# Optimization experiments

Measured on AMD Instinct MI355X. Metric: run time of the kernel, lower is better.

The kernel has to match this reference:

```python
import jax, jax.numpy as jnp
import numpy as np


def setup_inputs() -> dict:
    key = jax.random.key(0)
    k1, k2, k3, k4 = jax.random.split(key, 4)
    C, R = 64, 8  # channels, reduced = channels // 8
    B, D, H, W = 2, 16, 16, 16
    x = jax.random.normal(k1, (B, C, D, H, W), dtype=jnp.float32)
    # 1x1x1 Conv3d kernels are plain [out_ch, in_ch] matrices (no bias)
    Wq = jax.random.normal(k2, (R, C), dtype=jnp.float32) * (C ** -0.5)
    Wk = jax.random.normal(k3, (R, C), dtype=jnp.float32) * (C ** -0.5)
    Wv = jax.random.normal(k4, (C, C), dtype=jnp.float32) * (C ** -0.5)
    gamma = jnp.ones((1,), dtype=jnp.float32) * 0.5  # nonzero so output depends on attention
    return {"x": x, "Wq": Wq, "Wk": Wk, "Wv": Wv, "gamma": gamma}


def reference(x, Wq, Wk, Wv, gamma):
    b, c, d, h, w = x.shape
    n = d * h * w
    xf = x.astype(jnp.float32).reshape(b, c, n)        # [b, c, n]
    q = jnp.einsum('rc,bcn->bnr', Wq, xf)              # [b, n, r]
    k = jnp.einsum('rc,bcn->brn', Wk, xf)              # [b, r, n]
    scale = q.shape[-1] ** -0.5
    attn = jax.nn.softmax(jnp.einsum('bnr,brm->bnm', q, k) * scale, axis=-1)  # [b, n_q, n_k]
    v = jnp.einsum('oc,bcn->bon', Wv, xf)              # [b, c, n]
    # out = value @ attn^T : out[b,c,q] = sum_k v[b,c,k] * attn[b,q,k]
    out = jnp.einsum('bck,bqk->bcq', v, attn).reshape(b, c, d, h, w)
    return x + gamma.astype(x.dtype) * out.astype(x.dtype)
```

## Files before the change

### kernel.cpp

```cpp
#include <hip/hip_runtime.h>
#include <math.h>

#define BB 2
#define CC 64
#define NN 4096
#define SCALE 0.35355339059327373f
#define DEFER_THR 8.0f

typedef _Float16 f16x8 __attribute__((ext_vector_type(8)));
typedef _Float16 f16x4 __attribute__((ext_vector_type(4)));
typedef float f32x4 __attribute__((ext_vector_type(4)));
typedef float f32x4v __attribute__((ext_vector_type(4)));

__global__ __launch_bounds__(256) void proj_kernel(
    const float* __restrict__ x, const float* __restrict__ Wq,
    const float* __restrict__ Wk, _Float16* __restrict__ qh,
    _Float16* __restrict__ kh, _Float16* __restrict__ xp)
{
    const int t = (int)blockIdx.x * 256 + (int)threadIdx.x;

    if (t < 16384) {
        const int grp = t >> 13;
        const int p = t & 8191;
        const int b = p >> 12;
        const int n = p & (NN - 1);
        const float* xc0 = x + (size_t)b * CC * NN + n;
        float xc[CC];
#pragma unroll
        for (int c = 0; c < CC; ++c) xc[c] = xc0[(size_t)c * NN];

        const float* W = (grp == 0) ? Wq : Wk;
        float a[8];
#pragma unroll
        for (int j = 0; j < 8; ++j) a[j] = 0.f;
#pragma unroll
        for (int c = 0; c < CC; ++c) {
            const float xv = xc[c];
#pragma unroll
            for (int j = 0; j < 8; ++j)
                a[j] = fmaf(W[j * CC + c], xv, a[j]);
        }
        f16x8 o;
        if (grp == 0) {
#pragma unroll
            for (int j = 0; j < 8; ++j) o[j] = (_Float16)(a[j] * SCALE);
            *(f16x8*)(qh + (size_t)p * 8) = o;
        } else {
#pragma unroll
            for (int j = 0; j < 8; ++j) o[j] = (_Float16)a[j];
            *(f16x8*)(kh + (size_t)p * 8) = o;
        }
    } else {
        const int pt = t - 16384;
        const int b = pt >> 15;
        const int g = (pt >> 6) & 511;
        const int c = pt & 63;
        const float* src = x + ((size_t)(b * CC + c) * NN + g * 8);
        const float4 a0 = *(const float4*)(src);
        const float4 a1 = *(const float4*)(src + 4);
        f16x8 o;
        o[0] = (_Float16)a0.x; o[1] = (_Float16)a0.y;
        o[2] = (_Float16)a0.z; o[3] = (_Float16)a0.w;
        o[4] = (_Float16)a1.x; o[5] = (_Float16)a1.y;
        o[6] = (_Float16)a1.z; o[7] = (_Float16)a1.w;
        ((f16x8*)xp)[pt] = o;
    }
}

static __device__ inline f16x8 make_pf(const float* p8, int lg, int lc)
{
    union { f16x4 h; unsigned u[2]; } P0, P1;
#pragma unroll
    for (int v = 0; v < 4; ++v) {
        P0.h[v] = (_Float16)p8[v];
        P1.h[v] = (_Float16)p8[4 + v];
    }
    const int sA = (((2 * lg) & 3) << 4) + lc;
    const int sB = (((2 * lg + 1) & 3) << 4) + lc;
    const unsigned t00 = __shfl(P0.u[0], sA), t01 = __shfl(P0.u[1], sA);
    const unsigned t10 = __shfl(P1.u[0], sA), t11 = __shfl(P1.u[1], sA);
    const unsigned u00 = __shfl(P0.u[0], sB), u01 = __shfl(P0.u[1], sB);
    const unsigned u10 = __shfl(P1.u[0], sB), u11 = __shfl(P1.u[1], sB);
    const bool hi = (lg & 2) != 0;
    union { unsigned u[4]; f16x8 v; } PF;
    PF.u[0] = hi ? t10 : t00;
    PF.u[1] = hi ? t11 : t01;
    PF.u[2] = hi ? u10 : u00;
    PF.u[3] = hi ? u11 : u01;
    return PF.v;
}

__global__ __launch_bounds__(512) void attn_kernel(
    const _Float16* __restrict__ qh, const _Float16* __restrict__ kh,
    const _Float16* __restrict__ xp, const float* __restrict__ x,
    const float* __restrict__ Wv, const float* __restrict__ gamma,
    float* __restrict__ out)
{
    const int tid = (int)threadIdx.x;
    const int wid = tid >> 6;
    const int lane = tid & 63;
    const int lg = lane >> 4;
    const int lc = lane & 15;
    const int qi = (int)blockIdx.x & 255;
    const int b  = (int)blockIdx.x >> 8;
    const int q0 = qi * 16;

    __shared__ float sm_acc[8 * 64 * 17];
    __shared__ float sm_m[8][16];
    __shared__ float sm_l[8][16];
    __shared__ float zm[64][16];

    const f16x8 zf = {};
    const f32x4 z4 = {};

    f16x8 qfrag = zf;
    if (lg == 0)
        qfrag = *(const f16x8*)(qh + (size_t)(b * NN + q0 + lc) * 8);

    float m = -1e30f, l = 0.f;
    f32x4 acc0 = z4, acc1 = z4, acc2 = z4, acc3 = z4;

    const _Float16* khb = kh + (size_t)b * NN * 8;
    const _Float16* xpb = xp + (size_t)b * 512 * CC * 8;
    const int kbase = wid * 512;

#pragma unroll 2
    for (int ch = 0; ch < 8; ++ch) {
        const int k0 = kbase + ch * 64;

        f16x8 kf0 = zf, kf1 = zf, kf2 = zf, kf3 = zf;
        if (lg == 0) {
            kf0 = *(const f16x8*)(khb + (size_t)(k0 + lc) * 8);
            kf1 = *(const f16x8*)(khb + (size_t)(k0 + 16 + lc) * 8);
            kf2 = *(const f16x8*)(khb + (size_t)(k0 + 32 + lc) * 8);
            kf3 = *(const f16x8*)(khb + (size_t)(k0 + 48 + lc) * 8);
        }
        f32x4 s0 = __builtin_amdgcn_mfma_f32_16x16x32_f16(kf0, qfrag, z4, 0, 0, 0);
        f32x4 s1 = __builtin_amdgcn_mfma_f32_16x16x32_f16(kf1, qfrag, z4, 0, 0, 0);
        f32x4 s2 = __builtin_amdgcn_mfma_f32_16x16x32_f16(kf2, qfrag, z4, 0, 0, 0);
        f32x4 s3 = __builtin_amdgcn_mfma_f32_16x16x32_f16(kf3, qfrag, z4, 0, 0, 0);

        float cm = fmaxf(
            fmaxf(fmaxf(fmaxf(s0[0], s0[1]), fmaxf(s0[2], s0[3])),
                  fmaxf(fmaxf(s1[0], s1[1]), fmaxf(s1[2], s1[3]))),
            fmaxf(fmaxf(fmaxf(s2[0], s2[1]), fmaxf(s2[2], s2[3])),
                  fmaxf(fmaxf(s3[0], s3[1]), fmaxf(s3[2], s3[3]))));
        cm = fmaxf(cm, __shfl_xor(cm, 16));
        cm = fmaxf(cm, __shfl_xor(cm, 32));

        if (!__all(cm <= m + DEFER_THR)) {
            const float mnew = fmaxf(m, cm);
            const float alpha = __expf(m - mnew);
            m = mnew;
            l *= alpha;
            acc0 *= alpha; acc1 *= alpha; acc2 *= alpha; acc3 *= alpha;
        }

        float pr[16];
        float ls = 0.f;
#pragma unroll
        for (int v = 0; v < 4; ++v) { pr[v]      = __expf(s0[v] - m); ls += pr[v]; }
#pragma unroll
        for (int v = 0; v < 4; ++v) { pr[4 + v]  = __expf(s1[v] - m); ls += pr[4 + v]; }
#pragma unroll
        for (int v = 0; v < 4; ++v) { pr[8 + v]  = __expf(s2[v] - m); ls += pr[8 + v]; }
#pragma unroll
        for (int v = 0; v < 4; ++v) { pr[12 + v] = __expf(s3[v] - m); ls += pr[12 + v]; }
        ls += __shfl_xor(ls, 16);
        ls += __shfl_xor(ls, 32);
        l += ls;

        {
            const f16x8 PF = make_pf(pr, lg, lc);
            const _Float16* vg = xpb + (size_t)((k0 >> 3) + lg) * CC * 8;
            f16x8 v0 = *(const f16x8*)(vg + (0 * 16 + lc) * 8);
            f16x8 v1 = *(const f16x8*)(vg + (1 * 16 + lc) * 8);
            f16x8 v2 = *(const f16x8*)(vg + (2 * 16 + lc) * 8);
            f16x8 v3 = *(const f16x8*)(vg + (3 * 16 + lc) * 8);
            acc0 = __builtin_amdgcn_mfma_f32_16x16x32_f16(v0, PF, acc0, 0, 0, 0);
            acc1 = __builtin_amdgcn_mfma_f32_16x16x32_f16(v1, PF, acc1, 0, 0, 0);
            acc2 = __builtin_amdgcn_mfma_f32_16x16x32_f16(v2, PF, acc2, 0, 0, 0);
            acc3 = __builtin_amdgcn_mfma_f32_16x16x32_f16(v3, PF, acc3, 0, 0, 0);
        }
        {
            const f16x8 PF = make_pf(pr + 8, lg, lc);
            const _Float16* vg = xpb + (size_t)((k0 >> 3) + 4 + lg) * CC * 8;
            f16x8 v0 = *(const f16x8*)(vg + (0 * 16 + lc) * 8);
            f16x8 v1 = *(const f16x8*)(vg + (1 * 16 + lc) * 8);
            f16x8 v2 = *(const f16x8*)(vg + (2 * 16 + lc) * 8);
            f16x8 v3 = *(const f16x8*)(vg + (3 * 16 + lc) * 8);
            acc0 = __builtin_amdgcn_mfma_f32_16x16x32_f16(v0, PF, acc0, 0, 0, 0);
            acc1 = __builtin_amdgcn_mfma_f32_16x16x32_f16(v1, PF, acc1, 0, 0, 0);
            acc2 = __builtin_amdgcn_mfma_f32_16x16x32_f16(v2, PF, acc2, 0, 0, 0);
            acc3 = __builtin_amdgcn_mfma_f32_16x16x32_f16(v3, PF, acc3, 0, 0, 0);
        }
    }

    if (lane < 16) { sm_m[wid][lc] = m; sm_l[wid][lc] = l; }
    {
        float* sa = sm_acc + (size_t)wid * 64 * 17 + lc;
#pragma unroll
        for (int v = 0; v < 4; ++v) {
            sa[(0 * 16 + lg * 4 + v) * 17] = acc0[v];
            sa[(1 * 16 + lg * 4 + v) * 17] = acc1[v];
            sa[(2 * 16 + lg * 4 + v) * 17] = acc2[v];
            sa[(3 * 16 + lg * 4 + v) * 17] = acc3[v];
        }
    }
    __syncthreads();

    {
        const int c = tid >> 3;
        const int q2 = (tid & 7) * 2;
#pragma unroll
        for (int dq = 0; dq < 2; ++dq) {
            const int q = q2 + dq;
            float M = sm_m[0][q];
#pragma unroll
            for (int w = 1; w < 8; ++w) M = fmaxf(M, sm_m[w][q]);
            float L = 0.f, O = 0.f;
#pragma unroll
            for (int w = 0; w < 8; ++w) {
                const float e = __expf(sm_m[w][q] - M);
                L = fmaf(sm_l[w][q], e, L);
                O = fmaf(sm_acc[(w * 64 + c) * 17 + q], e, O);
            }
            zm[c][q] = O / L;
        }
    }
    __syncthreads();

    {
        const int c = tid >> 3;
        const int q2 = (tid & 7) * 2;
        const float* wr = Wv + c * 64;
        float o0 = 0.f, o1 = 0.f;
#pragma unroll
        for (int cc = 0; cc < 64; ++cc) {
            const float wv = wr[cc];
            o0 = fmaf(wv, zm[cc][q2],     o0);
            o1 = fmaf(wv, zm[cc][q2 + 1], o1);
        }
        const float g = gamma[0];
        const size_t oi = (size_t)b * CC * NN + (size_t)c * NN + q0 + q2;
        out[oi]     = fmaf(g, o0, x[oi]);
        out[oi + 1] = fmaf(g, o1, x[oi + 1]);
    }
}

extern "C" void kernel_launch(void* const* d_in, const int* in_sizes, int n_in,
                              void* d_out, int out_size, void* d_ws, size_t ws_size,
                              hipStream_t stream)
{
    const float* x     = (const float*)d_in[0];
    const float* Wq    = (const float*)d_in[1];
    const float* Wk    = (const float*)d_in[2];
    const float* Wv    = (const float*)d_in[3];
    const float* gamma = (const float*)d_in[4];
    float* out = (float*)d_out;

    char* ws = (char*)d_ws;
    _Float16* qh = (_Float16*)ws;
    _Float16* kh = qh + (size_t)BB * NN * 8;
    _Float16* xp = kh + (size_t)BB * NN * 8;

    hipLaunchKernelGGL(proj_kernel, dim3(320), dim3(256), 0, stream,
                       x, Wq, Wk, qh, kh, xp);
    hipLaunchKernelGGL(attn_kernel, dim3(BB * 256), dim3(512), 0, stream,
                       qh, kh, xp, x, Wv, gamma, out);
}
```

Baseline: 87.89 us.

## Fuse projection and attention kernels with a global atomic grid barrier

Merges the projection/convert kernel into the attention kernel. Each of 512 blocks first computes a slice of q/k projections and the fp16 copy of x, then all blocks meet at a spin-wait barrier on a global atomic counter before running attention. This removes one kernel launch and the gap between the two kernels. In exchange it needs a memset launch, relies on all 512 blocks being co-resident (launch_bounds 512,4) to avoid deadlock, and the projection work now runs on only 160 threads per block.

```diff
diff --git a/kernel.cpp b/kernel.cpp
--- a/kernel.cpp
+++ b/kernel.cpp
@@ -4,68 +4,13 @@
 #define BB 2
 #define CC 64
 #define NN 4096
+#define NBLK 512
 #define SCALE 0.35355339059327373f
 #define DEFER_THR 8.0f
 
 typedef _Float16 f16x8 __attribute__((ext_vector_type(8)));
 typedef _Float16 f16x4 __attribute__((ext_vector_type(4)));
 typedef float f32x4 __attribute__((ext_vector_type(4)));
-typedef float f32x4v __attribute__((ext_vector_type(4)));
-
-__global__ __launch_bounds__(256) void proj_kernel(
-    const float* __restrict__ x, const float* __restrict__ Wq,
-    const float* __restrict__ Wk, _Float16* __restrict__ qh,
-    _Float16* __restrict__ kh, _Float16* __restrict__ xp)
-{
-    const int t = (int)blockIdx.x * 256 + (int)threadIdx.x;
-
-    if (t < 16384) {
-        const int grp = t >> 13;
-        const int p = t & 8191;
-        const int b = p >> 12;
-        const int n = p & (NN - 1);
-        const float* xc0 = x + (size_t)b * CC * NN + n;
-        float xc[CC];
-#pragma unroll
-        for (int c = 0; c < CC; ++c) xc[c] = xc0[(size_t)c * NN];
-
-        const float* W = (grp == 0) ? Wq : Wk;
-        float a[8];
-#pragma unroll
-        for (int j = 0; j < 8; ++j) a[j] = 0.f;
-#pragma unroll
-        for (int c = 0; c < CC; ++c) {
-            const float xv = xc[c];
-#pragma unroll
-            for (int j = 0; j < 8; ++j)
-                a[j] = fmaf(W[j * CC + c], xv, a[j]);
-        }
-        f16x8 o;
-        if (grp == 0) {
-#pragma unroll
-            for (int j = 0; j < 8; ++j) o[j] = (_Float16)(a[j] * SCALE);
-            *(f16x8*)(qh + (size_t)p * 8) = o;
-        } else {
-#pragma unroll
-            for (int j = 0; j < 8; ++j) o[j] = (_Float16)a[j];
-            *(f16x8*)(kh + (size_t)p * 8) = o;
-        }
-    } else {
-        const int pt = t - 16384;
-        const int b = pt >> 15;
-        const int g = (pt >> 6) & 511;
-        const int c = pt & 63;
-        const float* src = x + ((size_t)(b * CC + c) * NN + g * 8);
-        const float4 a0 = *(const float4*)(src);
-        const float4 a1 = *(const float4*)(src + 4);
-        f16x8 o;
-        o[0] = (_Float16)a0.x; o[1] = (_Float16)a0.y;
-        o[2] = (_Float16)a0.z; o[3] = (_Float16)a0.w;
-        o[4] = (_Float16)a1.x; o[5] = (_Float16)a1.y;
-        o[6] = (_Float16)a1.z; o[7] = (_Float16)a1.w;
-        ((f16x8*)xp)[pt] = o;
-    }
-}
 
 static __device__ inline f16x8 make_pf(const float* p8, int lg, int lc)
 {
@@ -90,25 +35,90 @@
     return PF.v;
 }
 
-__global__ __launch_bounds__(512) void attn_kernel(
-    const _Float16* __restrict__ qh, const _Float16* __restrict__ kh,
-    const _Float16* __restrict__ xp, const float* __restrict__ x,
-    const float* __restrict__ Wv, const float* __restrict__ gamma,
-    float* __restrict__ out)
+__global__ __launch_bounds__(512, 4) void fused_kernel(
+    const float* __restrict__ x, const float* __restrict__ Wq,
+    const float* __restrict__ Wk, const float* __restrict__ Wv,
+    const float* __restrict__ gamma, float* __restrict__ out,
+    unsigned* __restrict__ ctr, _Float16* __restrict__ qh,
+    _Float16* __restrict__ kh, _Float16* __restrict__ xp)
 {
     const int tid = (int)threadIdx.x;
+    const int bid = (int)blockIdx.x;
+
+    __shared__ float sm_acc[8 * 64 * 17];
+    __shared__ float sm_m[8][16];
+    __shared__ float sm_l[8][16];
+    __shared__ float zm[64][16];
+
+    if (tid < 32) {
+        const int v = tid * 512 + bid;
+        const int grp = v >> 13;
+        const int p = v & 8191;
+        const int b = p >> 12;
+        const int n = p & (NN - 1);
+        const float* xc0 = x + (size_t)b * CC * NN + n;
+        float xc[CC];
+#pragma unroll
+        for (int c = 0; c < CC; ++c) xc[c] = xc0[(size_t)c * NN];
+
+        const float* W = (grp == 0) ? Wq : Wk;
+        float a[8];
+#pragma unroll
+        for (int j = 0; j < 8; ++j) a[j] = 0.f;
+#pragma unroll
+        for (int c = 0; c < CC; ++c) {
+            const float xv = xc[c];
+#pragma unroll
+            for (int j = 0; j < 8; ++j)
+                a[j] = fmaf(W[j * CC + c], xv, a[j]);
+        }
+        f16x8 o;
+        if (grp == 0) {
+#pragma unroll
+            for (int j = 0; j < 8; ++j) o[j] = (_Float16)(a[j] * SCALE);
+            *(f16x8*)(qh + (size_t)p * 8) = o;
+        } else {
+#pragma unroll
+            for (int j = 0; j < 8; ++j) o[j] = (_Float16)a[j];
+            *(f16x8*)(kh + (size_t)p * 8) = o;
+        }
+    } else if (tid < 160) {
+        const int pt = bid * 128 + (tid - 32);
+        const int b = pt >> 15;
+        const int g = (pt >> 6) & 511;
+        const int c = pt & 63;
+        const float* src = x + ((size_t)(b * CC + c) * NN + g * 8);
+        const float4 a0 = *(const float4*)(src);
+        const float4 a1 = *(const float4*)(src + 4);
+        f16x8 o;
+        o[0] = (_Float16)a0.x; o[1] = (_Float16)a0.y;
+        o[2] = (_Float16)a0.z; o[3] = (_Float16)a0.w;
+        o[4] = (_Float16)a1.x; o[5] = (_Float16)a1.y;
+        o[6] = (_Float16)a1.z; o[7] = (_Float16)a1.w;
+        ((f16x8*)xp)[pt] = o;
+    }
+
+    __threadfence();
+    __syncthreads();
+    if (tid == 0) {
+        atomicAdd(ctr, 1u);
+        int guard = 0;
+        while (__hip_atomic_load(ctr, __ATOMIC_ACQUIRE,
+                                 __HIP_MEMORY_SCOPE_AGENT) < (unsigned)NBLK &&
+               guard < (1 << 20)) {
+            __builtin_amdgcn_s_sleep(64);
+            ++guard;
+        }
+    }
+    __syncthreads();
+
     const int wid = tid >> 6;
     const int lane = tid & 63;
     const int lg = lane >> 4;
     const int lc = lane & 15;
-    const int qi = (int)blockIdx.x & 255;
-    const int b  = (int)blockIdx.x >> 8;
+    const int qi = bid & 255;
+    const int b  = bid >> 8;
     const int q0 = qi * 16;
-
-    __shared__ float sm_acc[8 * 64 * 17];
-    __shared__ float sm_m[8][16];
-    __shared__ float sm_l[8][16];
-    __shared__ float zm[64][16];
 
     const f16x8 zf = {};
     const f32x4 z4 = {};
@@ -260,12 +270,12 @@
     float* out = (float*)d_out;
 
     char* ws = (char*)d_ws;
-    _Float16* qh = (_Float16*)ws;
+    unsigned* ctr = (unsigned*)ws;
+    _Float16* qh = (_Float16*)(ws + 256);
     _Float16* kh = qh + (size_t)BB * NN * 8;
     _Float16* xp = kh + (size_t)BB * NN * 8;
 
-    hipLaunchKernelGGL(proj_kernel, dim3(320), dim3(256), 0, stream,
-                       x, Wq, Wk, qh, kh, xp);
-    hipLaunchKernelGGL(attn_kernel, dim3(BB * 256), dim3(512), 0, stream,
-                       qh, kh, xp, x, Wv, gamma, out);
+    hipMemsetAsync(ctr, 0, 4, stream);
+    hipLaunchKernelGGL(fused_kernel, dim3(NBLK), dim3(512), 0, stream,
+                       x, Wq, Wk, Wv, gamma, out, ctr, qh, kh, xp);
 }
```

Result: slower. 209.2 us (+138.0%).
